# Kernel tuning notes

Hardware: AMD Instinct MI355X
Metric: run time of the kernel (lower is better)

The kernel has to match this reference:

```python
import jax, jax.numpy as jnp
import numpy as np

B, S, HID = 2, 2048, 1024
NH, HD = 16, 64
EPS = 1e-12


def setup_inputs() -> dict:
    key = jax.random.key(0)
    ks = jax.random.split(key, 6)
    w_scale = 1.0 / np.sqrt(HID)
    return {
        "hidden_states": jax.random.normal(ks[0], (B, S, HID), dtype=jnp.float32),
        "attention_mask": jnp.ones((B, S), dtype=jnp.float32),
        "Wq": jax.random.normal(ks[1], (HID, HID), dtype=jnp.float32) * w_scale,
        "bq": jnp.zeros((HID,), dtype=jnp.float32),
        "Wk": jax.random.normal(ks[2], (HID, HID), dtype=jnp.float32) * w_scale,
        "bk": jnp.zeros((HID,), dtype=jnp.float32),
        "Wv": jax.random.normal(ks[3], (HID, HID), dtype=jnp.float32) * w_scale,
        "bv": jnp.zeros((HID,), dtype=jnp.float32),
        "Wd": jax.random.normal(ks[4], (HID, HID), dtype=jnp.float32) * w_scale,
        "bd": jnp.zeros((HID,), dtype=jnp.float32),
        "ln_gamma": jnp.ones((HID,), dtype=jnp.float32),
        "ln_beta": jnp.zeros((HID,), dtype=jnp.float32),
    }


def _heads(x):  # [B,S,HID] -> [B,NH,S,HD]
    return x.reshape(B, S, NH, HD).transpose(0, 2, 1, 3)


def reference(hidden_states, attention_mask, Wq, bq, Wk, bk, Wv, bv, Wd, bd, ln_gamma, ln_beta):
    # pre-LayerNorm
    mu = jnp.mean(hidden_states, axis=-1, keepdims=True)
    var = jnp.mean(jnp.square(hidden_states - mu), axis=-1, keepdims=True)
    h = (hidden_states - mu) * jax.lax.rsqrt(var + EPS) * ln_gamma + ln_beta

    q = _heads(h @ Wq.T + bq)  # [B,NH,S,HD]
    k = _heads(h @ Wk.T + bk)
    v = _heads(h @ Wv.T + bv)

    # additive mask: -1000 * (1 - mask), broadcast over heads and query pos
    add_mask = -1000.0 * (1.0 - attention_mask)[:, None, None, :]  # [B,1,1,S]

    # scale applied symmetrically to q and k: sqrt(sqrt(HD)) each
    scale = np.sqrt(np.sqrt(HD)).astype(np.float32)
    scores = jnp.einsum("bhqd,bhkd->bhqk", q / scale, k / scale) + add_mask
    probs = jax.nn.softmax(scores, axis=-1)  # dropout p=0 -> identity
    ctx = jnp.einsum("bhqk,bhkd->bhqd", probs, v)  # [B,NH,S,HD]

    ctx = ctx.transpose(0, 2, 1, 3).reshape(B, S, HID)
    return ctx @ Wd.T + bd
```

## Files before the change

kernel.cpp:

```cpp
#include <hip/hip_runtime.h>
#include <hip/hip_bf16.h>
#include <math.h>

#define BATCH 2
#define SEQ   2048
#define HID   1024
#define NH    16
#define HD    64
#define MROWS (BATCH * SEQ)
#define VSTR  4160

typedef unsigned short u16;
typedef short bf16x8 __attribute__((ext_vector_type(8)));
typedef short bf16x4 __attribute__((ext_vector_type(4)));
typedef float f32x4  __attribute__((ext_vector_type(4)));

#define LOG2E 1.4426950408889634f
#define C2    (0.125f * LOG2E)
#define M2F   23.083120f

static __device__ __forceinline__ u16 f2bf(float f) {
    union { float f; unsigned int u; } v; v.f = f;
    unsigned int r = (v.u + 0x7FFF + ((v.u >> 16) & 1)) >> 16;
    return (u16)r;
}

static __device__ __forceinline__ unsigned int pk_bf16(float a, float b) {
    union { __hip_bfloat162 h; unsigned int u; } r;
    float2 f; f.x = a; f.y = b;
    r.h = __float22bfloat162_rn(f);
    return r.u;
}

static __device__ __forceinline__ f32x4 mfma16(bf16x8 a, bf16x8 b, f32x4 c) {
    return __builtin_amdgcn_mfma_f32_16x16x32_bf16(a, b, c, 0, 0, 0);
}

static __device__ __forceinline__ f32x4 mfma16k16(bf16x4 a, bf16x4 b, f32x4 c) {
#if __has_builtin(__builtin_amdgcn_mfma_f32_16x16x16bf16_1k)
    return __builtin_amdgcn_mfma_f32_16x16x16bf16_1k(a, b, c, 0, 0, 0);
#else
    bf16x8 a8 = {a[0], a[1], a[2], a[3], 0, 0, 0, 0};
    bf16x8 b8 = {b[0], b[1], b[2], b[3], 0, 0, 0, 0};
    return __builtin_amdgcn_mfma_f32_16x16x32_bf16(a8, b8, c, 0, 0, 0);
#endif
}

static __device__ __forceinline__ void ldsload16(const void* g, void* l) {
    __builtin_amdgcn_global_load_lds(
        (const __attribute__((address_space(1))) void*)(unsigned long long)(uintptr_t)g,
        (__attribute__((address_space(3))) void*)(unsigned int)(uintptr_t)l,
        16, 0, 0);
}

__global__ __launch_bounds__(256) void prep_kernel(const float* __restrict__ x,
                                                   const float* __restrict__ gamma,
                                                   const float* __restrict__ beta,
                                                   u16* __restrict__ h,
                                                   const float* __restrict__ w0,
                                                   const float* __restrict__ w1,
                                                   const float* __restrict__ w2,
                                                   const float* __restrict__ w3,
                                                   u16* o0, u16* o1, u16* o2, u16* o3,
                                                   const float* __restrict__ maskg,
                                                   float* __restrict__ m2g)
{
    __shared__ float red[8];
    const int t = threadIdx.x;
    if (blockIdx.x >= 8192) {
        const int idx = ((blockIdx.x - 8192) * 256 + t) * 4;
        const float4 m = *(const float4*)(maskg + idx);
        float4 o;
        o.x = fmaf(-1000.0f * (1.0f - m.x), LOG2E, -M2F);
        o.y = fmaf(-1000.0f * (1.0f - m.y), LOG2E, -M2F);
        o.z = fmaf(-1000.0f * (1.0f - m.z), LOG2E, -M2F);
        o.w = fmaf(-1000.0f * (1.0f - m.w), LOG2E, -M2F);
        *(float4*)(m2g + idx) = o;
        return;
    }
    if (blockIdx.x < 4096) {
        const int blk = blockIdx.x;
        const int which = blk >> 10;
        const int lb = blk & 1023;
        const float* src = which == 0 ? w0 : which == 1 ? w1 : which == 2 ? w2 : w3;
        u16* dst = which == 0 ? o0 : which == 1 ? o1 : which == 2 ? o2 : o3;
        const int idx = (lb * 256 + t) * 4;
        const float4 f = *(const float4*)(src + idx);
        union { u16 s[4]; uint2 v; } p;
        p.s[0] = f2bf(f.x); p.s[1] = f2bf(f.y); p.s[2] = f2bf(f.z); p.s[3] = f2bf(f.w);
        *(uint2*)(dst + idx) = p.v;
        return;
    }
    const int row = blockIdx.x - 4096;
    const float4 xv = ((const float4*)(x + (size_t)row * HID))[t];
    float s  = xv.x + xv.y + xv.z + xv.w;
    float ss = xv.x * xv.x + xv.y * xv.y + xv.z * xv.z + xv.w * xv.w;
#pragma unroll
    for (int off = 32; off > 0; off >>= 1) {
        s  += __shfl_down(s, off);
        ss += __shfl_down(ss, off);
    }
    const int wid = t >> 6;
    if ((t & 63) == 0) { red[wid] = s; red[4 + wid] = ss; }
    __syncthreads();
    s  = red[0] + red[1] + red[2] + red[3];
    ss = red[4] + red[5] + red[6] + red[7];
    const float mu   = s * (1.0f / HID);
    const float var  = ss * (1.0f / HID) - mu * mu;
    const float rstd = rsqrtf(var + 1e-12f);
    const float4 g  = ((const float4*)gamma)[t];
    const float4 bb = ((const float4*)beta)[t];
    union { u16 s[4]; uint2 v; } p;
    p.s[0] = f2bf((xv.x - mu) * rstd * g.x + bb.x);
    p.s[1] = f2bf((xv.y - mu) * rstd * g.y + bb.y);
    p.s[2] = f2bf((xv.z - mu) * rstd * g.z + bb.z);
    p.s[3] = f2bf((xv.w - mu) * rstd * g.w + bb.w);
    ((uint2*)(h + (size_t)row * HID))[t] = p.v;
}

static __device__ __forceinline__ void gemm_core(const u16* __restrict__ A,
                                                 const u16* __restrict__ B,
                                                 int K, int bm, int bn,
                                                 u16* As, u16* Bs,
                                                 int wave, int lane,
                                                 f32x4 acc[4][4])
{
    const int l15  = lane & 15;
    const int quad = lane >> 4;
    const int wm = (wave >> 1) * 64;
    const int wn = (wave & 1) * 64;

    const int c1 = wave * 64 + lane;
    const int c2 = c1 + 256;
    const u16* A1 = A + (size_t)(bm + (c1 >> 2)) * K + (c1 & 3) * 8;
    const u16* A2 = A + (size_t)(bm + (c2 >> 2)) * K + (c2 & 3) * 8;
    const u16* B1 = B + (size_t)(bn + (c1 >> 2)) * K + (c1 & 3) * 8;
    const u16* B2 = B + (size_t)(bn + (c2 >> 2)) * K + (c2 & 3) * 8;
    const int o1 = wave * 512;
    const int o2 = 2048 + wave * 512;

    ldsload16(A1, As + o1);
    ldsload16(A2, As + o2);
    ldsload16(B1, Bs + o1);
    ldsload16(B2, Bs + o2);

    const int nstep = K >> 5;
    for (int i = 0; i < nstep; i++) {
        __syncthreads();
        const int cb = (i & 1) * 4096;
        if (i + 1 < nstep) {
            const int nb = ((i + 1) & 1) * 4096;
            const int k0 = (i + 1) * 32;
            ldsload16(A1 + k0, As + nb + o1);
            ldsload16(A2 + k0, As + nb + o2);
            ldsload16(B1 + k0, Bs + nb + o1);
            ldsload16(B2 + k0, Bs + nb + o2);
        }
        bf16x8 af[4], bfr[4];
#pragma unroll
        for (int mt = 0; mt < 4; mt++)
            af[mt] = *(const bf16x8*)&As[cb + (wm + mt * 16 + l15) * 32 + quad * 8];
#pragma unroll
        for (int nt = 0; nt < 4; nt++)
            bfr[nt] = *(const bf16x8*)&Bs[cb + (wn + nt * 16 + l15) * 32 + quad * 8];
#pragma unroll
        for (int mt = 0; mt < 4; mt++)
#pragma unroll
            for (int nt = 0; nt < 4; nt++)
                acc[mt][nt] = mfma16(af[mt], bfr[nt], acc[mt][nt]);
    }
}

__global__ __launch_bounds__(256) void qkv_gemm(const u16* __restrict__ h,
                                                const u16* __restrict__ wq,
                                                const u16* __restrict__ wk,
                                                const u16* __restrict__ wv,
                                                const float* __restrict__ bq,
                                                const float* __restrict__ bk,
                                                const float* __restrict__ bv,
                                                u16* __restrict__ qo,
                                                u16* __restrict__ ko,
                                                u16* __restrict__ vo)
{
    __shared__ u16 As[8192];
    __shared__ u16 Bs[8192];
    const int blk  = blockIdx.x;
    const int wave = threadIdx.x >> 6;
    const int lane = threadIdx.x & 63;
    const int l15  = lane & 15;
    const int quad = lane >> 4;
    const int wm = (wave >> 1) * 64;
    const int wn = (wave & 1) * 64;

    f32x4 acc[4][4];
#pragma unroll
    for (int mt = 0; mt < 4; mt++)
#pragma unroll
        for (int nt = 0; nt < 4; nt++) acc[mt][nt] = (f32x4)0.0f;

    if (blk < 512) {
        const u16* W     = (blk < 256) ? wq : wk;
        const float* bia = (blk < 256) ? bq : bk;
        u16* out         = (blk < 256) ? qo : ko;
        const int local = blk & 255;
        const int bm = (local >> 3) * 128;
        const int bn = (local & 7) * 128;
        gemm_core(h, W, HID, bm, bn, As, Bs, wave, lane, acc);

        float bv4[4];
#pragma unroll
        for (int nt = 0; nt < 4; nt++) bv4[nt] = bia[bn + wn + nt * 16 + l15];
#pragma unroll
        for (int mt = 0; mt < 4; mt++)
#pragma unroll
            for (int r = 0; r < 4; r++) {
                const int m  = bm + wm + mt * 16 + quad * 4 + r;
                const int bI = m >> 11;
                const int sI = m & (SEQ - 1);
#pragma unroll
                for (int nt = 0; nt < 4; nt++) {
                    const int n  = bn + wn + nt * 16 + l15;
                    const int hh = n >> 6;
                    const int d  = n & 63;
                    out[(((size_t)(bI * NH + hh) * SEQ + sI) << 6) + d] =
                        f2bf(acc[mt][nt][r] + bv4[nt]);
                }
            }
    } else {
        const int local = blk - 512;
        const int bm = (local & 7) * 128;
        const int bn = (local >> 3) * 128;
        gemm_core(wv, h, HID, bm, bn, As, Bs, wave, lane, acc);

#pragma unroll
        for (int mt = 0; mt < 4; mt++) {
            const f32x4 bm4 = *(const f32x4*)&bv[bm + wm + mt * 16 + quad * 4];
#pragma unroll
            for (int r = 0; r < 4; r++) {
                const int row = bm + wm + mt * 16 + quad * 4 + r;
#pragma unroll
                for (int nt = 0; nt < 4; nt++) {
                    const int col = bn + wn + nt * 16 + l15;
                    vo[(size_t)row * VSTR + col] = f2bf(acc[mt][nt][r] + bm4[r]);
                }
            }
        }
    }
}

__global__ __launch_bounds__(256) void out_gemm(const u16* __restrict__ ctx,
                                                const u16* __restrict__ wd,
                                                const float* __restrict__ bd,
                                                float* __restrict__ out)
{
    __shared__ u16 As[8192];
    __shared__ u16 Bs[8192];
    const int blk  = blockIdx.x;
    const int wave = threadIdx.x >> 6;
    const int lane = threadIdx.x & 63;
    const int l15  = lane & 15;
    const int quad = lane >> 4;
    const int wm = (wave >> 1) * 64;
    const int wn = (wave & 1) * 64;
    const int bm = (blk >> 3) * 128;
    const int bn = (blk & 7) * 128;

    f32x4 acc[4][4];
#pragma unroll
    for (int mt = 0; mt < 4; mt++)
#pragma unroll
        for (int nt = 0; nt < 4; nt++) acc[mt][nt] = (f32x4)0.0f;

    gemm_core(ctx, wd, HID, bm, bn, As, Bs, wave, lane, acc);

    float bv4[4];
#pragma unroll
    for (int nt = 0; nt < 4; nt++) bv4[nt] = bd[bn + wn + nt * 16 + l15];
#pragma unroll
    for (int mt = 0; mt < 4; mt++)
#pragma unroll
        for (int r = 0; r < 4; r++) {
            const int m = bm + wm + mt * 16 + quad * 4 + r;
#pragma unroll
            for (int nt = 0; nt < 4; nt++) {
                const int n = bn + wn + nt * 16 + l15;
                out[(size_t)m * HID + n] = acc[mt][nt][r] + bv4[nt];
            }
        }
}

__global__ __launch_bounds__(256) void attn_mfma(const u16* __restrict__ qb,
                                                 const u16* __restrict__ kb,
                                                 const u16* __restrict__ vtb,
                                                 const float* __restrict__ m2g,
                                                 u16* __restrict__ ctx)
{
    __shared__ __align__(16) char smem[66560];

    const int t    = threadIdx.x;
    const int wave = t >> 6;
    const int lane = t & 63;
    const int l15  = lane & 15;
    const int quad = lane >> 4;

    const int bh = blockIdx.x & 31;
    const int qt = blockIdx.x >> 5;
    const int b  = bh >> 4;
    const int hh = bh & 15;
    const int q0 = qt * 64;

    const size_t headoff = (size_t)(b * NH + hh) * SEQ * HD;
    const u16* kbase = kb + headoff;
    const u16* vbase = vtb + (size_t)(hh * HD) * VSTR + b * SEQ;
    const float* m2b = m2g + b * SEQ;

    char* Ksw  = smem + wave * 16384;
    char* Vtsw = Ksw + 8192;

    bf16x8 Qf[4][2];
#pragma unroll
    for (int nt = 0; nt < 4; nt++)
#pragma unroll
        for (int ks2 = 0; ks2 < 2; ks2++)
            Qf[nt][ks2] = *(const bf16x8*)(qb + headoff +
                (size_t)(q0 + nt * 16 + l15) * HD + ks2 * 32 + quad * 8);

    f32x4 O[4][4];
#pragma unroll
    for (int mt = 0; mt < 4; mt++)
#pragma unroll
        for (int nt = 0; nt < 4; nt++) O[mt][nt] = (f32x4)0.0f;
    float ls4[4] = {0.0f, 0.0f, 0.0f, 0.0f};

    const int srow = lane >> 3;
    const int lcol = (lane & 7) ^ srow;
    const int swk0 = ((quad)     ^ (l15 & 7)) * 8;
    const int swk1 = ((quad + 4) ^ (l15 & 7)) * 8;
    const int cbase = wave * 512;

#pragma unroll
    for (int g = 0; g < 8; g++) {
        ldsload16(kbase + (size_t)(cbase + g * 8 + srow) * HD + lcol * 8, Ksw + g * 1024);
        ldsload16(vbase + (size_t)(g * 8 + srow) * VSTR + cbase + lcol * 8, Vtsw + g * 1024);
    }

    for (int j = 0; j < 8; j++) {
        const int c0 = cbase + j * 64;
        asm volatile("s_waitcnt vmcnt(0)" ::: "memory");

        bf16x8 Ka[4][2];
#pragma unroll
        for (int ks = 0; ks < 4; ks++) {
            const u16* Kp = (const u16*)Ksw + (ks * 16 + l15) * 64;
            Ka[ks][0] = *(const bf16x8*)(Kp + swk0);
            Ka[ks][1] = *(const bf16x8*)(Kp + swk1);
        }
        bf16x4 Va[4][4];
#pragma unroll
        for (int mt2 = 0; mt2 < 4; mt2++) {
            const u16* Vp = (const u16*)Vtsw + (mt2 * 16 + l15) * 64 + ((quad & 1) << 2);
#pragma unroll
            for (int ks = 0; ks < 4; ks++)
                Va[mt2][ks] = *(const bf16x4*)(Vp +
                    ((((ks << 1) | (quad >> 1)) ^ (l15 & 7)) << 3));
        }
        asm volatile("s_waitcnt lgkmcnt(0)" ::: "memory");

        if (j + 1 < 8) {
            const int cn = c0 + 64;
#pragma unroll
            for (int g = 0; g < 8; g++) {
                ldsload16(kbase + (size_t)(cn + g * 8 + srow) * HD + lcol * 8, Ksw + g * 1024);
                ldsload16(vbase + (size_t)(g * 8 + srow) * VSTR + cn + lcol * 8, Vtsw + g * 1024);
            }
        }

        bf16x4 Pk[4][4];
#pragma unroll
        for (int ks = 0; ks < 4; ks++) {
            f32x4 St[4];
#pragma unroll
            for (int nt = 0; nt < 4; nt++) {
                f32x4 a = (f32x4)0.0f;
                a = mfma16(Ka[ks][0], Qf[nt][0], a);
                a = mfma16(Ka[ks][1], Qf[nt][1], a);
                St[nt] = a;
            }
            const f32x4 mv = *(const f32x4*)(m2b + c0 + ks * 16 + quad * 4);
#pragma unroll
            for (int nt = 0; nt < 4; nt++) {
                const float p0 = __builtin_amdgcn_exp2f(fmaf(St[nt][0], C2, mv[0]));
                const float p1 = __builtin_amdgcn_exp2f(fmaf(St[nt][1], C2, mv[1]));
                const float p2 = __builtin_amdgcn_exp2f(fmaf(St[nt][2], C2, mv[2]));
                const float p3 = __builtin_amdgcn_exp2f(fmaf(St[nt][3], C2, mv[3]));
                ls4[nt] += (p0 + p1) + (p2 + p3);
                union { unsigned int u[2]; bf16x4 v; } pk;
                pk.u[0] = pk_bf16(p0, p1);
                pk.u[1] = pk_bf16(p2, p3);
                Pk[ks][nt] = pk.v;
            }
        }

#pragma unroll
        for (int mt2 = 0; mt2 < 4; mt2++)
#pragma unroll
            for (int nt = 0; nt < 4; nt++) {
                f32x4 acc = O[mt2][nt];
#pragma unroll
                for (int ks = 0; ks < 4; ks++)
                    acc = mfma16k16(Va[mt2][ks], Pk[ks][nt], acc);
                O[mt2][nt] = acc;
            }
    }

#pragma unroll
    for (int nt = 0; nt < 4; nt++) {
        ls4[nt] += __shfl_xor(ls4[nt], 16);
        ls4[nt] += __shfl_xor(ls4[nt], 32);
    }

    {
        float* Opart = (float*)(smem + wave * 16384);
#pragma unroll
        for (int mt2 = 0; mt2 < 4; mt2++)
#pragma unroll
            for (int nt = 0; nt < 4; nt++)
                *(f32x4*)(Opart + ((mt2 * 4 + nt) * 64 + lane) * 4) = O[mt2][nt];
        float* lsb = (float*)(smem + 65536);
        if (lane < 16) {
#pragma unroll
            for (int nt = 0; nt < 4; nt++)
                lsb[wave * 64 + nt * 16 + lane] = ls4[nt];
        }
    }
    __syncthreads();

    f32x4 Of[4];
    {
        const float* lsb = (const float*)(smem + 65536);
#pragma unroll
        for (int nt = 0; nt < 4; nt++) {
            const int k = wave * 4 + nt;
            f32x4 s = *(const f32x4*)(smem + 0 * 16384 + (k * 64 + lane) * 16);
            s = s + *(const f32x4*)(smem + 1 * 16384 + (k * 64 + lane) * 16);
            s = s + *(const f32x4*)(smem + 2 * 16384 + (k * 64 + lane) * 16);
            s = s + *(const f32x4*)(smem + 3 * 16384 + (k * 64 + lane) * 16);
            const int q = nt * 16 + l15;
            const float lt = lsb[q] + lsb[64 + q] + lsb[128 + q] + lsb[192 + q];
            Of[nt] = s * (1.0f / lt);
        }
    }
    __syncthreads();

    {
        float* Ot = (float*)smem;
#pragma unroll
        for (int nt = 0; nt < 4; nt++)
            *(f32x4*)(Ot + (nt * 16 + l15) * 68 + wave * 16 + quad * 4) = Of[nt];
    }
    __syncthreads();

    {
        const float* Ot = (const float*)smem;
        const int ql  = t >> 2;
        const int seg = t & 3;
        const float* srcp = Ot + ql * 68 + seg * 16;
        u16* dstp = ctx + (size_t)(b * SEQ + q0 + ql) * HID + hh * 64 + seg * 16;
#pragma unroll
        for (int jj = 0; jj < 2; jj++) {
            union { u16 s[8]; uint4 v; } p;
#pragma unroll
            for (int i = 0; i < 8; i++) p.s[i] = f2bf(srcp[jj * 8 + i]);
            *(uint4*)(dstp + jj * 8) = p.v;
        }
    }
}

extern "C" void kernel_launch(void* const* d_in, const int* in_sizes, int n_in,
                              void* d_out, int out_size, void* d_ws, size_t ws_size,
                              hipStream_t stream)
{
    const float* hs    = (const float*)d_in[0];
    const float* mask  = (const float*)d_in[1];
    const float* Wq    = (const float*)d_in[2];
    const float* bq    = (const float*)d_in[3];
    const float* Wk    = (const float*)d_in[4];
    const float* bk    = (const float*)d_in[5];
    const float* Wv    = (const float*)d_in[6];
    const float* bv    = (const float*)d_in[7];
    const float* Wd    = (const float*)d_in[8];
    const float* bd    = (const float*)d_in[9];
    const float* gamma = (const float*)d_in[10];
    const float* beta  = (const float*)d_in[11];
    float* out = (float*)d_out;

    const size_t NE = (size_t)MROWS * HID;
    u16* ws   = (u16*)d_ws;
    u16* h    = ws;
    u16* qbb  = ws + NE;
    u16* kbb  = qbb + NE;
    u16* vtb  = kbb + NE;
    u16* ctxb = vtb + (size_t)HID * VSTR;
    u16* wqb  = ctxb + NE;
    u16* wkb  = wqb + HID * HID;
    u16* wvb  = wkb + HID * HID;
    u16* wdb  = wvb + HID * HID;
    float* m2 = (float*)(wdb + HID * HID);

    prep_kernel<<<8196, 256, 0, stream>>>(hs, gamma, beta, h,
                                          Wq, Wk, Wv, Wd, wqb, wkb, wvb, wdb,
                                          mask, m2);

    qkv_gemm<<<768, 256, 0, stream>>>(h, wqb, wkb, wvb, bq, bk, bv, qbb, kbb, vtb);

    attn_mfma<<<1024, 256, 0, stream>>>(qbb, kbb, vtb, m2, ctxb);

    out_gemm<<<256, 256, 0, stream>>>(ctxb, wdb, bd, out);
}
```

Baseline: 234.9 us.

## Split attention work by query rows across waves with shared double-buffered K/V tiles

```diff
diff --git a/kernel.cpp b/kernel.cpp
--- a/kernel.cpp
+++ b/kernel.cpp
@@ -295,7 +295,7 @@
                                                  const float* __restrict__ m2g,
                                                  u16* __restrict__ ctx)
 {
-    __shared__ __align__(16) char smem[66560];
+    __shared__ __align__(16) char smem[34816];
 
     const int t    = threadIdx.x;
     const int wave = t >> 6;
@@ -307,93 +307,76 @@
     const int qt = blockIdx.x >> 5;
     const int b  = bh >> 4;
     const int hh = bh & 15;
-    const int q0 = qt * 64;
+    const int q0 = qt * 128;
 
     const size_t headoff = (size_t)(b * NH + hh) * SEQ * HD;
     const u16* kbase = kb + headoff;
     const u16* vbase = vtb + (size_t)(hh * HD) * VSTR + b * SEQ;
     const float* m2b = m2g + b * SEQ;
 
-    char* Ksw  = smem + wave * 16384;
-    char* Vtsw = Ksw + 8192;
-
-    bf16x8 Qf[4][2];
-#pragma unroll
-    for (int nt = 0; nt < 4; nt++)
+    bf16x8 Qf[2][2];
+#pragma unroll
+    for (int nt = 0; nt < 2; nt++)
 #pragma unroll
         for (int ks2 = 0; ks2 < 2; ks2++)
             Qf[nt][ks2] = *(const bf16x8*)(qb + headoff +
-                (size_t)(q0 + nt * 16 + l15) * HD + ks2 * 32 + quad * 8);
-
-    f32x4 O[4][4];
-#pragma unroll
-    for (int mt = 0; mt < 4; mt++)
-#pragma unroll
-        for (int nt = 0; nt < 4; nt++) O[mt][nt] = (f32x4)0.0f;
-    float ls4[4] = {0.0f, 0.0f, 0.0f, 0.0f};
+                (size_t)(q0 + wave * 32 + nt * 16 + l15) * HD + ks2 * 32 + quad * 8);
+
+    f32x4 O[4][2];
+#pragma unroll
+    for (int mt2 = 0; mt2 < 4; mt2++)
+#pragma unroll
+        for (int nt = 0; nt < 2; nt++) O[mt2][nt] = (f32x4)0.0f;
+    float ls2[2] = {0.0f, 0.0f};
 
     const int srow = lane >> 3;
     const int lcol = (lane & 7) ^ srow;
     const int swk0 = ((quad)     ^ (l15 & 7)) * 8;
     const int swk1 = ((quad + 4) ^ (l15 & 7)) * 8;
-    const int cbase = wave * 512;
-
-#pragma unroll
-    for (int g = 0; g < 8; g++) {
-        ldsload16(kbase + (size_t)(cbase + g * 8 + srow) * HD + lcol * 8, Ksw + g * 1024);
-        ldsload16(vbase + (size_t)(g * 8 + srow) * VSTR + cbase + lcol * 8, Vtsw + g * 1024);
-    }
-
-    for (int j = 0; j < 8; j++) {
-        const int c0 = cbase + j * 64;
-        asm volatile("s_waitcnt vmcnt(0)" ::: "memory");
-
-        bf16x8 Ka[4][2];
+    const int g0 = wave * 2;
+
+    ldsload16(kbase + (size_t)(g0 * 8 + srow) * HD + lcol * 8,           smem + g0 * 1024);
+    ldsload16(kbase + (size_t)(g0 * 8 + 8 + srow) * HD + lcol * 8,       smem + g0 * 1024 + 1024);
+    ldsload16(vbase + (size_t)(g0 * 8 + srow) * VSTR + lcol * 8,         smem + 16384 + g0 * 1024);
+    ldsload16(vbase + (size_t)(g0 * 8 + 8 + srow) * VSTR + lcol * 8,     smem + 16384 + g0 * 1024 + 1024);
+
+    for (int i = 0; i < 32; i++) {
+        __syncthreads();
+        const int c0 = i * 64;
+        const u16* Ks  = (const u16*)(smem + (i & 1) * 8192);
+        const u16* Vts = (const u16*)(smem + 16384 + (i & 1) * 8192);
+        if (i + 1 < 32) {
+            const int cn = c0 + 64;
+            char* nbK = smem + ((i + 1) & 1) * 8192;
+            char* nbV = smem + 16384 + ((i + 1) & 1) * 8192;
+            ldsload16(kbase + (size_t)(cn + g0 * 8 + srow) * HD + lcol * 8,       nbK + g0 * 1024);
+            ldsload16(kbase + (size_t)(cn + g0 * 8 + 8 + srow) * HD + lcol * 8,   nbK + g0 * 1024 + 1024);
+            ldsload16(vbase + (size_t)(g0 * 8 + srow) * VSTR + cn + lcol * 8,     nbV + g0 * 1024);
+            ldsload16(vbase + (size_t)(g0 * 8 + 8 + srow) * VSTR + cn + lcol * 8, nbV + g0 * 1024 + 1024);
+        }
+
+        bf16x4 Pk[4][2];
 #pragma unroll
         for (int ks = 0; ks < 4; ks++) {
-            const u16* Kp = (const u16*)Ksw + (ks * 16 + l15) * 64;
-            Ka[ks][0] = *(const bf16x8*)(Kp + swk0);
-            Ka[ks][1] = *(const bf16x8*)(Kp + swk1);
-        }
-        bf16x4 Va[4][4];
-#pragma unroll
-        for (int mt2 = 0; mt2 < 4; mt2++) {
-            const u16* Vp = (const u16*)Vtsw + (mt2 * 16 + l15) * 64 + ((quad & 1) << 2);
-#pragma unroll
-            for (int ks = 0; ks < 4; ks++)
-                Va[mt2][ks] = *(const bf16x4*)(Vp +
-                    ((((ks << 1) | (quad >> 1)) ^ (l15 & 7)) << 3));
-        }
-        asm volatile("s_waitcnt lgkmcnt(0)" ::: "memory");
-
-        if (j + 1 < 8) {
-            const int cn = c0 + 64;
-#pragma unroll
-            for (int g = 0; g < 8; g++) {
-                ldsload16(kbase + (size_t)(cn + g * 8 + srow) * HD + lcol * 8, Ksw + g * 1024);
-                ldsload16(vbase + (size_t)(g * 8 + srow) * VSTR + cn + lcol * 8, Vtsw + g * 1024);
-            }
-        }
-
-        bf16x4 Pk[4][4];
-#pragma unroll
-        for (int ks = 0; ks < 4; ks++) {
-            f32x4 St[4];
-#pragma unroll
-            for (int nt = 0; nt < 4; nt++) {
+            const int rb = (ks * 16 + l15) * 64;
+            const bf16x8 ka0 = *(const bf16x8*)&Ks[rb + swk0];
+            const bf16x8 ka1 = *(const bf16x8*)&Ks[rb + swk1];
+            f32x4 St[2];
+#pragma unroll
+            for (int nt = 0; nt < 2; nt++) {
                 f32x4 a = (f32x4)0.0f;
-                a = mfma16(Ka[ks][0], Qf[nt][0], a);
-                a = mfma16(Ka[ks][1], Qf[nt][1], a);
+                a = mfma16(ka0, Qf[nt][0], a);
+                a = mfma16(ka1, Qf[nt][1], a);
                 St[nt] = a;
             }
             const f32x4 mv = *(const f32x4*)(m2b + c0 + ks * 16 + quad * 4);
 #pragma unroll
-            for (int nt = 0; nt < 4; nt++) {
+            for (int nt = 0; nt < 2; nt++) {
                 const float p0 = __builtin_amdgcn_exp2f(fmaf(St[nt][0], C2, mv[0]));
                 const float p1 = __builtin_amdgcn_exp2f(fmaf(St[nt][1], C2, mv[1]));
                 const float p2 = __builtin_amdgcn_exp2f(fmaf(St[nt][2], C2, mv[2]));
                 const float p3 = __builtin_amdgcn_exp2f(fmaf(St[nt][3], C2, mv[3]));
-                ls4[nt] += (p0 + p1) + (p2 + p3);
+                ls2[nt] += (p0 + p1) + (p2 + p3);
                 union { unsigned int u[2]; bf16x4 v; } pk;
                 pk.u[0] = pk_bf16(p0, p1);
                 pk.u[1] = pk_bf16(p2, p3);
@@ -402,76 +385,53 @@
         }
 
 #pragma unroll
-        for (int mt2 = 0; mt2 < 4; mt2++)
-#pragma unroll
-            for (int nt = 0; nt < 4; nt++) {
+        for (int mt2 = 0; mt2 < 4; mt2++) {
+            const u16* Vp = Vts + (mt2 * 16 + l15) * 64 + ((quad & 1) << 2);
+            bf16x4 Va[4];
+#pragma unroll
+            for (int ks = 0; ks < 4; ks++)
+                Va[ks] = *(const bf16x4*)(Vp +
+                    ((((ks << 1) | (quad >> 1)) ^ (l15 & 7)) << 3));
+#pragma unroll
+            for (int nt = 0; nt < 2; nt++) {
                 f32x4 acc = O[mt2][nt];
 #pragma unroll
                 for (int ks = 0; ks < 4; ks++)
-                    acc = mfma16k16(Va[mt2][ks], Pk[ks][nt], acc);
+                    acc = mfma16k16(Va[ks], Pk[ks][nt], acc);
                 O[mt2][nt] = acc;
             }
-    }
-
-#pragma unroll
-    for (int nt = 0; nt < 4; nt++) {
-        ls4[nt] += __shfl_xor(ls4[nt], 16);
-        ls4[nt] += __shfl_xor(ls4[nt], 32);
-    }
-
+        }
+    }
+
+#pragma unroll
+    for (int nt = 0; nt < 2; nt++) {
+        ls2[nt] += __shfl_xor(ls2[nt], 16);
+        ls2[nt] += __shfl_xor(ls2[nt], 32);
+    }
+    const float linv0 = 1.0f / ls2[0];
+    const float linv1 = 1.0f / ls2[1];
+
+    __syncthreads();
+    float* Ot = (float*)smem + wave * (32 * 68);
+#pragma unroll
+    for (int mt2 = 0; mt2 < 4; mt2++)
+#pragma unroll
+        for (int nt = 0; nt < 2; nt++) {
+            const f32x4 v = O[mt2][nt] * (nt ? linv1 : linv0);
+            *(f32x4*)(Ot + (nt * 16 + l15) * 68 + mt2 * 16 + quad * 4) = v;
+        }
     {
-        float* Opart = (float*)(smem + wave * 16384);
-#pragma unroll
-        for (int mt2 = 0; mt2 < 4; mt2++)
-#pragma unroll
-            for (int nt = 0; nt < 4; nt++)
-                *(f32x4*)(Opart + ((mt2 * 4 + nt) * 64 + lane) * 4) = O[mt2][nt];
-        float* lsb = (float*)(smem + 65536);
-        if (lane < 16) {
-#pragma unroll
-            for (int nt = 0; nt < 4; nt++)
-                lsb[wave * 64 + nt * 16 + lane] = ls4[nt];
-        }
-    }
-    __syncthreads();
-
-    f32x4 Of[4];
-    {
-        const float* lsb = (const float*)(smem + 65536);
-#pragma unroll
-        for (int nt = 0; nt < 4; nt++) {
-            const int k = wave * 4 + nt;
-            f32x4 s = *(const f32x4*)(smem + 0 * 16384 + (k * 64 + lane) * 16);
-            s = s + *(const f32x4*)(smem + 1 * 16384 + (k * 64 + lane) * 16);
-            s = s + *(const f32x4*)(smem + 2 * 16384 + (k * 64 + lane) * 16);
-            s = s + *(const f32x4*)(smem + 3 * 16384 + (k * 64 + lane) * 16);
-            const int q = nt * 16 + l15;
-            const float lt = lsb[q] + lsb[64 + q] + lsb[128 + q] + lsb[192 + q];
-            Of[nt] = s * (1.0f / lt);
-        }
-    }
-    __syncthreads();
-
-    {
-        float* Ot = (float*)smem;
-#pragma unroll
-        for (int nt = 0; nt < 4; nt++)
-            *(f32x4*)(Ot + (nt * 16 + l15) * 68 + wave * 16 + quad * 4) = Of[nt];
-    }
-    __syncthreads();
-
-    {
-        const float* Ot = (const float*)smem;
-        const int ql  = t >> 2;
-        const int seg = t & 3;
-        const float* srcp = Ot + ql * 68 + seg * 16;
-        u16* dstp = ctx + (size_t)(b * SEQ + q0 + ql) * HID + hh * 64 + seg * 16;
-#pragma unroll
-        for (int jj = 0; jj < 2; jj++) {
+        const int ql   = lane >> 1;
+        const int half = lane & 1;
+        const float* srcp = Ot + ql * 68 + half * 32;
+        u16* dstp = ctx + (size_t)(b * SEQ + q0 + wave * 32 + ql) * HID
+                        + hh * 64 + half * 32;
+#pragma unroll
+        for (int j = 0; j < 4; j++) {
             union { u16 s[8]; uint4 v; } p;
 #pragma unroll
-            for (int i = 0; i < 8; i++) p.s[i] = f2bf(srcp[jj * 8 + i]);
-            *(uint4*)(dstp + jj * 8) = p.v;
+            for (int ii = 0; ii < 8; ii++) p.s[ii] = f2bf(srcp[j * 8 + ii]);
+            *(uint4*)(dstp + j * 8) = p.v;
         }
     }
 }
@@ -513,7 +473,7 @@
 
     qkv_gemm<<<768, 256, 0, stream>>>(h, wqb, wkb, wvb, bq, bk, bv, qbb, kbb, vtb);
 
-    attn_mfma<<<1024, 256, 0, stream>>>(qbb, kbb, vtb, m2, ctxb);
+    attn_mfma<<<512, 256, 0, stream>>>(qbb, kbb, vtb, m2, ctxb);
 
     out_gemm<<<256, 256, 0, stream>>>(ctxb, wdb, bd, out);
 }
```

New measurement: 223.9 us. -4.7%, faster.
